# Kernel optimization log

Hardware: AMD Instinct MI355X
Metric: run time of the kernel (lower is better)

The kernel has to match this reference:

```python
import jax, jax.numpy as jnp
import numpy as np

N = 50000      # nodes
E = 800000     # edges (avg degree 16)
DN = 128       # in_node_feats (== out_feats)
DE = 64        # in_edge_feats
DO = 128       # out_feats


def setup_inputs() -> dict:
    key = jax.random.key(0)
    k1, k2, k3, k4, k5 = jax.random.split(key, 5)
    node_feats = jax.random.normal(k1, (N, DN), dtype=jnp.float32)
    edge_feats = jax.random.normal(k2, (E, DE), dtype=jnp.float32)
    src = jax.random.randint(k3, (E,), 0, N, dtype=jnp.int64) if jax.config.jax_enable_x64 else jax.random.randint(k3, (E,), 0, N).astype(jnp.int32)
    dst = jax.random.randint(k4, (E,), 0, N).astype(src.dtype)
    # nn.Linear(2*DN+DE, DO): weight [DO, 2*DN+DE], bias [DO]
    W = jax.random.normal(k5, (DO, 2 * DN + DE), dtype=jnp.float32) * 0.05
    b = jnp.zeros((DO,), dtype=jnp.float32)
    return {"node_feats": node_feats, "edge_feats": edge_feats, "W": W, "b": b, "src": src, "dst": dst}


def reference(node_feats, edge_feats, W, b, src, dst):
    # message: linear(cat([h_src, h_dst, e_f])) per edge -> [E, DO]
    msg_in = jnp.concatenate([node_feats[src], node_feats[dst], edge_feats], axis=1)  # [E, 2*DN+DE]
    mail = msg_in @ W.T + b                                                           # [E, DO]
    # scatter-mean at destination nodes (DGL mailbox mean)
    sums = jax.ops.segment_sum(mail, dst, num_segments=N)                             # [N, DO]
    deg = jax.ops.segment_sum(jnp.ones((mail.shape[0],), mail.dtype), dst, num_segments=N)  # [N]
    mean = sums / jnp.maximum(deg, 1.0)[:, None]
    # nodes with no incoming messages keep their original h (DGL update_all semantics)
    h = jnp.where(deg[:, None] > 0, mean, node_feats)
    # activation (relu); dropout is identity in eval / p=0
    return jax.nn.relu(h)
```

## Files before the change

### kernel.cpp

```cpp
#include <hip/hip_runtime.h>

#define DN 128
#define DE 64
#define DO 128
#define DIN 320
#define LDX 72
#define PAD 64

typedef short bf16x8 __attribute__((ext_vector_type(8)));
typedef float f32x4 __attribute__((ext_vector_type(4)));
typedef unsigned long long u64;

__device__ inline unsigned short f2bf(float f) {
    unsigned u = __builtin_bit_cast(unsigned, f);
    u = (u + 0x7fffu + ((u >> 16) & 1u)) >> 16;
    return (unsigned short)u;
}
__device__ inline unsigned pk2(float a, float b) {
    return (unsigned)f2bf(a) | ((unsigned)f2bf(b) << 16);
}
__device__ inline float bf2f(unsigned short h) {
    unsigned u = ((unsigned)h) << 16;
    return __builtin_bit_cast(float, u);
}

__global__ __launch_bounds__(256) void convert_kernel(
    const float* __restrict__ W, const float* __restrict__ nf,
    unsigned short* __restrict__ Wbf, unsigned short* __restrict__ nfbf,
    int nW4, int n4tot)
{
    int i = blockIdx.x * 256 + threadIdx.x;
    if (i >= n4tot) return;
    const float* sp;
    unsigned short* dp;
    int j;
    if (i < nW4) { sp = W;  dp = Wbf;  j = i; }
    else         { sp = nf; dp = nfbf; j = i - nW4; }
    const float4 v = *(const float4*)&sp[(size_t)j * 4];
    u64 val = (u64)pk2(v.x, v.y) | ((u64)pk2(v.z, v.w) << 32);
    *(u64*)&dp[(size_t)j * 4] = val;
}

__global__ __launch_bounds__(256) void fill_kernel(
    const int* __restrict__ dst, const int* __restrict__ src,
    int* __restrict__ cursor, u64* __restrict__ es, int E)
{
    int e = blockIdx.x * 256 + threadIdx.x;
    if (e >= E) return;
    int d = dst[e];
    int s = src[e];
    int pos = atomicAdd(&cursor[d], 1);
    if (pos < PAD)
        es[(size_t)d * PAD + pos] = (u64)(unsigned)e | ((u64)(unsigned)s << 32);
}

__global__ __launch_bounds__(256) void gather_kernel(
    const unsigned short* __restrict__ nfbf, const float* __restrict__ ef,
    const u64* __restrict__ es, const int* __restrict__ cursor,
    unsigned short* __restrict__ agg_src_bf,
    unsigned short* __restrict__ agg_edge_bf, int N)
{
    const int wave = threadIdx.x >> 6;
    const int lane = threadIdx.x & 63;
    const int v = blockIdx.x * 4 + wave;
    if (v >= N) return;

    const int cnt = min(cursor[v], PAD);

    const int g = lane >> 4;
    const int q = lane & 15;

    float accN[8];
#pragma unroll
    for (int j = 0; j < 8; ++j) accN[j] = 0.f;
    f32x4 accE = {0.f, 0.f, 0.f, 0.f};

    int e_l = 0, s_l = 0;
    if (lane < cnt) {
        u64 p = __builtin_nontemporal_load(&es[(size_t)v * PAD + lane]);
        e_l = (int)(unsigned)(p & 0xffffffffu);
        s_l = (int)(unsigned)(p >> 32);
    }
    for (int i = 0; i < cnt; i += 16) {
        const int s0 = __shfl(s_l, i + g, 64);
        const int s1 = __shfl(s_l, i + 4 + g, 64);
        const int s2 = __shfl(s_l, i + 8 + g, 64);
        const int s3 = __shfl(s_l, i + 12 + g, 64);
        const int e0 = __shfl(e_l, i + g, 64);
        const int e1 = __shfl(e_l, i + 4 + g, 64);
        const int e2 = __shfl(e_l, i + 8 + g, 64);
        const int e3 = __shfl(e_l, i + 12 + g, 64);
        bf16x8 n0 = *(const bf16x8*)&nfbf[(size_t)s0 * DN + q * 8];
        bf16x8 n1 = *(const bf16x8*)&nfbf[(size_t)s1 * DN + q * 8];
        bf16x8 n2 = *(const bf16x8*)&nfbf[(size_t)s2 * DN + q * 8];
        bf16x8 n3 = *(const bf16x8*)&nfbf[(size_t)s3 * DN + q * 8];
        f32x4 f0 = __builtin_nontemporal_load((const f32x4*)&ef[(size_t)e0 * DE + q * 4]);
        f32x4 f1 = __builtin_nontemporal_load((const f32x4*)&ef[(size_t)e1 * DE + q * 4]);
        f32x4 f2 = __builtin_nontemporal_load((const f32x4*)&ef[(size_t)e2 * DE + q * 4]);
        f32x4 f3 = __builtin_nontemporal_load((const f32x4*)&ef[(size_t)e3 * DE + q * 4]);
        if (i + g < cnt) {
#pragma unroll
            for (int j = 0; j < 8; ++j) accN[j] += bf2f((unsigned short)n0[j]);
            accE += f0;
        }
        if (i + 4 + g < cnt) {
#pragma unroll
            for (int j = 0; j < 8; ++j) accN[j] += bf2f((unsigned short)n1[j]);
            accE += f1;
        }
        if (i + 8 + g < cnt) {
#pragma unroll
            for (int j = 0; j < 8; ++j) accN[j] += bf2f((unsigned short)n2[j]);
            accE += f2;
        }
        if (i + 12 + g < cnt) {
#pragma unroll
            for (int j = 0; j < 8; ++j) accN[j] += bf2f((unsigned short)n3[j]);
            accE += f3;
        }
    }

#pragma unroll
    for (int j = 0; j < 8; ++j) {
        accN[j] += __shfl_xor(accN[j], 16, 64);
        accN[j] += __shfl_xor(accN[j], 32, 64);
    }
#pragma unroll
    for (int j = 0; j < 4; ++j) {
        accE[j] += __shfl_xor(accE[j], 16, 64);
        accE[j] += __shfl_xor(accE[j], 32, 64);
    }

    const float inv = (cnt > 0) ? (1.0f / (float)cnt) : 0.0f;
    if (g == 0) {
        uint4 val;
        val.x = pk2(accN[0] * inv, accN[1] * inv);
        val.y = pk2(accN[2] * inv, accN[3] * inv);
        val.z = pk2(accN[4] * inv, accN[5] * inv);
        val.w = pk2(accN[6] * inv, accN[7] * inv);
        *(uint4*)&agg_src_bf[(size_t)v * DN + q * 8] = val;
    } else if (g == 1) {
        u64 val = (u64)pk2(accE[0] * inv, accE[1] * inv) |
                  ((u64)pk2(accE[2] * inv, accE[3] * inv) << 32);
        *(u64*)&agg_edge_bf[(size_t)v * DE + q * 4] = val;
    }
}

__global__ __launch_bounds__(256) void finalize_kernel(
    const float* __restrict__ nf, const unsigned short* __restrict__ nfbf,
    const unsigned short* __restrict__ Wbf, const float* __restrict__ b,
    const unsigned short* __restrict__ agg_src_bf,
    const unsigned short* __restrict__ agg_edge_bf,
    const int* __restrict__ cursor, float* __restrict__ out, int N)
{
    __shared__ unsigned short Ws[DO * LDX];
    __shared__ unsigned short Xs[64 * LDX];
    __shared__ float bs[DO];
    __shared__ int degs[64];

    const int tid = threadIdx.x;
    const int lane = tid & 63;
    const int w = tid >> 6;
    const int node0 = blockIdx.x * 64;

    if (tid < DO) bs[tid] = b[tid];
    if (tid < 64) {
        int v = node0 + tid;
        degs[tid] = (v < N) ? cursor[v] : 0;
    }

    f32x4 acc[8];
#pragma unroll
    for (int r = 0; r < 8; ++r) acc[r] = (f32x4){0.f, 0.f, 0.f, 0.f};

    for (int c = 0; c < 5; ++c) {
        const int k0 = c * 64;
        __syncthreads();
#pragma unroll
        for (int it = 0; it < 8; ++it) {
            int i4 = tid + it * 256;
            int o = i4 >> 4;
            int kk = (i4 & 15) * 4;
            *(u64*)&Ws[o * LDX + kk] = *(const u64*)&Wbf[o * DIN + k0 + kk];
        }
#pragma unroll
        for (int it = 0; it < 4; ++it) {
            int i4 = tid + it * 256;
            int n = i4 >> 4;
            int kk = (i4 & 15) * 4;
            int v = node0 + n;
            u64 val = 0;
            if (v < N) {
                if (c < 2) {
                    val = *(const u64*)&agg_src_bf[(size_t)v * DN + k0 + kk];
                } else if (c < 4) {
                    val = *(const u64*)&nfbf[(size_t)v * DN + (c - 2) * 64 + kk];
                } else {
                    val = *(const u64*)&agg_edge_bf[(size_t)v * DE + kk];
                }
            }
            *(u64*)&Xs[n * LDX + kk] = val;
        }
        __syncthreads();

        const int xrow = 16 * w + (lane & 15);
        const int kgrp = (lane >> 4) * 8;
#pragma unroll
        for (int t = 0; t < 2; ++t) {
            bf16x8 a = *(const bf16x8*)&Xs[xrow * LDX + t * 32 + kgrp];
#pragma unroll
            for (int r = 0; r < 8; ++r) {
                bf16x8 bw = *(const bf16x8*)&Ws[(16 * r + (lane & 15)) * LDX + t * 32 + kgrp];
                acc[r] = __builtin_amdgcn_mfma_f32_16x16x32_bf16(a, bw, acc[r], 0, 0, 0);
            }
        }
    }

    const int col = lane & 15;
#pragma unroll
    for (int r = 0; r < 8; ++r) {
        const int o = 16 * r + col;
        const float bo = bs[o];
#pragma unroll
        for (int reg = 0; reg < 4; ++reg) {
            const int n = 16 * w + (lane >> 4) * 4 + reg;
            const int v = node0 + n;
            if (v >= N) continue;
            float val = (degs[n] > 0) ? (acc[r][reg] + bo) : nf[(size_t)v * DN + o];
            out[(size_t)v * DO + o] = fmaxf(val, 0.0f);
        }
    }
}

extern "C" void kernel_launch(void* const* d_in, const int* in_sizes, int n_in,
                              void* d_out, int out_size, void* d_ws, size_t ws_size,
                              hipStream_t stream)
{
    const float* nf  = (const float*)d_in[0];
    const float* ef  = (const float*)d_in[1];
    const float* W   = (const float*)d_in[2];
    const float* b   = (const float*)d_in[3];
    const int*   src = (const int*)d_in[4];
    const int*   dst = (const int*)d_in[5];
    float* out = (float*)d_out;

    const int N = in_sizes[0] / DN;
    const int E = in_sizes[4];

    char* p = (char*)d_ws;
    int* cursor = (int*)p;  p += (size_t)N * 4;
    p = (char*)(((uintptr_t)p + 15) & ~(uintptr_t)15);
    u64* es     = (u64*)p;  p += (size_t)N * PAD * 8;
    unsigned short* agg_src_bf  = (unsigned short*)p;  p += (size_t)N * DN * 2;
    unsigned short* agg_edge_bf = (unsigned short*)p;  p += (size_t)N * DE * 2;
    unsigned short* nfbf        = (unsigned short*)p;  p += (size_t)N * DN * 2;
    unsigned short* Wbf         = (unsigned short*)p;

    (void)hipMemsetAsync(cursor, 0, (size_t)N * sizeof(int), stream);

    const int nW4 = DO * DIN / 4;
    const int n4tot = nW4 + N * DN / 4;
    convert_kernel<<<(n4tot + 255) / 256, 256, 0, stream>>>(W, nf, Wbf, nfbf, nW4, n4tot);

    const int eb = (E + 255) / 256;
    fill_kernel<<<eb, 256, 0, stream>>>(dst, src, cursor, es, E);

    const int gb = (N + 3) / 4;
    gather_kernel<<<gb, 256, 0, stream>>>(nfbf, ef, es, cursor,
                                          agg_src_bf, agg_edge_bf, N);

    const int nb = (N + 63) / 64;
    finalize_kernel<<<nb, 256, 0, stream>>>(nf, nfbf, Wbf, b, agg_src_bf,
                                            agg_edge_bf, cursor, out, N);
}
```

Before: 151.1 us.

## Gather source node features from an FP8 copy and fold cursor reset into convert

```diff
diff --git a/kernel.cpp b/kernel.cpp
--- a/kernel.cpp
+++ b/kernel.cpp
@@ -23,22 +23,41 @@
     unsigned u = ((unsigned)h) << 16;
     return __builtin_bit_cast(float, u);
 }
+__device__ inline unsigned f2fp8(float f) {
+    unsigned u = __builtin_bit_cast(unsigned, f * 0x1p-120f);
+    unsigned s = (u >> 24) & 0x80u;
+    u &= 0x7fffffffu;
+    unsigned r = (u + 0x7ffffu + ((u >> 20) & 1u)) >> 20;
+    if (r > 0x7eu) r = 0x7eu;
+    return s | r;
+}
+__device__ inline float fp8_acc(unsigned b, float acc) {
+    unsigned u = ((b & 0x80u) << 24) | ((b & 0x7fu) << 20);
+    return fmaf(__builtin_bit_cast(float, u), 0x1p120f, acc);
+}
 
 __global__ __launch_bounds__(256) void convert_kernel(
     const float* __restrict__ W, const float* __restrict__ nf,
     unsigned short* __restrict__ Wbf, unsigned short* __restrict__ nfbf,
-    int nW4, int n4tot)
+    unsigned char* __restrict__ nf8, int* __restrict__ cursor,
+    int nW4, int n4tot, int N)
 {
     int i = blockIdx.x * 256 + threadIdx.x;
+    if (i < N) cursor[i] = 0;
     if (i >= n4tot) return;
-    const float* sp;
-    unsigned short* dp;
-    int j;
-    if (i < nW4) { sp = W;  dp = Wbf;  j = i; }
-    else         { sp = nf; dp = nfbf; j = i - nW4; }
-    const float4 v = *(const float4*)&sp[(size_t)j * 4];
-    u64 val = (u64)pk2(v.x, v.y) | ((u64)pk2(v.z, v.w) << 32);
-    *(u64*)&dp[(size_t)j * 4] = val;
+    if (i < nW4) {
+        const float4 v = *(const float4*)&W[(size_t)i * 4];
+        u64 val = (u64)pk2(v.x, v.y) | ((u64)pk2(v.z, v.w) << 32);
+        *(u64*)&Wbf[(size_t)i * 4] = val;
+    } else {
+        int j = i - nW4;
+        const float4 v = *(const float4*)&nf[(size_t)j * 4];
+        u64 val = (u64)pk2(v.x, v.y) | ((u64)pk2(v.z, v.w) << 32);
+        *(u64*)&nfbf[(size_t)j * 4] = val;
+        unsigned p8 = f2fp8(v.x) | (f2fp8(v.y) << 8) |
+                      (f2fp8(v.z) << 16) | (f2fp8(v.w) << 24);
+        *(unsigned*)&nf8[(size_t)j * 4] = p8;
+    }
 }
 
 __global__ __launch_bounds__(256) void fill_kernel(
@@ -55,7 +74,7 @@
 }
 
 __global__ __launch_bounds__(256) void gather_kernel(
-    const unsigned short* __restrict__ nfbf, const float* __restrict__ ef,
+    const unsigned char* __restrict__ nf8, const float* __restrict__ ef,
     const u64* __restrict__ es, const int* __restrict__ cursor,
     unsigned short* __restrict__ agg_src_bf,
     unsigned short* __restrict__ agg_edge_bf, int N)
@@ -90,32 +109,32 @@
         const int e1 = __shfl(e_l, i + 4 + g, 64);
         const int e2 = __shfl(e_l, i + 8 + g, 64);
         const int e3 = __shfl(e_l, i + 12 + g, 64);
-        bf16x8 n0 = *(const bf16x8*)&nfbf[(size_t)s0 * DN + q * 8];
-        bf16x8 n1 = *(const bf16x8*)&nfbf[(size_t)s1 * DN + q * 8];
-        bf16x8 n2 = *(const bf16x8*)&nfbf[(size_t)s2 * DN + q * 8];
-        bf16x8 n3 = *(const bf16x8*)&nfbf[(size_t)s3 * DN + q * 8];
+        u64 n0 = *(const u64*)&nf8[(size_t)s0 * DN + q * 8];
+        u64 n1 = *(const u64*)&nf8[(size_t)s1 * DN + q * 8];
+        u64 n2 = *(const u64*)&nf8[(size_t)s2 * DN + q * 8];
+        u64 n3 = *(const u64*)&nf8[(size_t)s3 * DN + q * 8];
         f32x4 f0 = __builtin_nontemporal_load((const f32x4*)&ef[(size_t)e0 * DE + q * 4]);
         f32x4 f1 = __builtin_nontemporal_load((const f32x4*)&ef[(size_t)e1 * DE + q * 4]);
         f32x4 f2 = __builtin_nontemporal_load((const f32x4*)&ef[(size_t)e2 * DE + q * 4]);
         f32x4 f3 = __builtin_nontemporal_load((const f32x4*)&ef[(size_t)e3 * DE + q * 4]);
         if (i + g < cnt) {
 #pragma unroll
-            for (int j = 0; j < 8; ++j) accN[j] += bf2f((unsigned short)n0[j]);
+            for (int j = 0; j < 8; ++j) accN[j] = fp8_acc((unsigned)(n0 >> (j * 8)) & 0xffu, accN[j]);
             accE += f0;
         }
         if (i + 4 + g < cnt) {
 #pragma unroll
-            for (int j = 0; j < 8; ++j) accN[j] += bf2f((unsigned short)n1[j]);
+            for (int j = 0; j < 8; ++j) accN[j] = fp8_acc((unsigned)(n1 >> (j * 8)) & 0xffu, accN[j]);
             accE += f1;
         }
         if (i + 8 + g < cnt) {
 #pragma unroll
-            for (int j = 0; j < 8; ++j) accN[j] += bf2f((unsigned short)n2[j]);
+            for (int j = 0; j < 8; ++j) accN[j] = fp8_acc((unsigned)(n2 >> (j * 8)) & 0xffu, accN[j]);
             accE += f2;
         }
         if (i + 12 + g < cnt) {
 #pragma unroll
-            for (int j = 0; j < 8; ++j) accN[j] += bf2f((unsigned short)n3[j]);
+            for (int j = 0; j < 8; ++j) accN[j] = fp8_acc((unsigned)(n3 >> (j * 8)) & 0xffu, accN[j]);
             accE += f3;
         }
     }
@@ -227,7 +246,7 @@
             const int v = node0 + n;
             if (v >= N) continue;
             float val = (degs[n] > 0) ? (acc[r][reg] + bo) : nf[(size_t)v * DN + o];
-            out[(size_t)v * DO + o] = fmaxf(val, 0.0f);
+            __builtin_nontemporal_store(fmaxf(val, 0.0f), &out[(size_t)v * DO + o]);
         }
     }
 }
@@ -254,19 +273,19 @@
     unsigned short* agg_src_bf  = (unsigned short*)p;  p += (size_t)N * DN * 2;
     unsigned short* agg_edge_bf = (unsigned short*)p;  p += (size_t)N * DE * 2;
     unsigned short* nfbf        = (unsigned short*)p;  p += (size_t)N * DN * 2;
+    unsigned char*  nf8         = (unsigned char*)p;   p += (size_t)N * DN;
     unsigned short* Wbf         = (unsigned short*)p;
-
-    (void)hipMemsetAsync(cursor, 0, (size_t)N * sizeof(int), stream);
 
     const int nW4 = DO * DIN / 4;
     const int n4tot = nW4 + N * DN / 4;
-    convert_kernel<<<(n4tot + 255) / 256, 256, 0, stream>>>(W, nf, Wbf, nfbf, nW4, n4tot);
+    convert_kernel<<<(n4tot + 255) / 256, 256, 0, stream>>>(
+        W, nf, Wbf, nfbf, nf8, cursor, nW4, n4tot, N);
 
     const int eb = (E + 255) / 256;
     fill_kernel<<<eb, 256, 0, stream>>>(dst, src, cursor, es, E);
 
     const int gb = (N + 3) / 4;
-    gather_kernel<<<gb, 256, 0, stream>>>(nfbf, ef, es, cursor,
+    gather_kernel<<<gb, 256, 0, stream>>>(nf8, ef, es, cursor,
                                           agg_src_bf, agg_edge_bf, N);
 
     const int nb = (N + 63) / 64;
```

New measurement: 133.7 us. -11.5%, faster.
